# Kernel optimization log

Hardware: AMD Instinct MI355X
Metric: run time of the kernel (lower is better)

Reference implementation:

```python
import jax, jax.numpy as jnp
import numpy as np

N, E = 20000, 320000
H1, C1 = 8, 128   # gat1 heads/out
H2, C2 = 1, 128   # gat2 heads/out
D_IN = 768
NEG_SLOPE = 0.2
BN_EPS = 1e-5


def setup_inputs() -> dict:
    key = jax.random.key(0)
    ks = jax.random.split(key, 16)
    def rn(k, shape, fan):
        return jax.random.normal(k, shape, dtype=jnp.float32) / np.sqrt(fan)
    x = jax.random.normal(ks[0], (N, D_IN), dtype=jnp.float32)
    edge_index = jax.random.randint(ks[1], (2, E), 0, N, dtype=jnp.int64)
    return {
        "x": x,
        "edge_index": edge_index,
        "W1": rn(ks[2], (D_IN, H1 * C1), D_IN),
        "att_src1": rn(ks[3], (H1, C1), C1),
        "att_dst1": rn(ks[4], (H1, C1), C1),
        "b1": jnp.zeros((H1 * C1,), jnp.float32),
        "W2": rn(ks[5], (H1 * C1, H2 * C2), H1 * C1),
        "att_src2": rn(ks[6], (H2, C2), C2),
        "att_dst2": rn(ks[7], (H2, C2), C2),
        "b2": jnp.zeros((C2,), jnp.float32),
        "g1": jnp.ones((H1 * C1,), jnp.float32),
        "be1": jnp.zeros((H1 * C1,), jnp.float32),
        "g2": jnp.ones((C2,), jnp.float32),
        "be2": jnp.zeros((C2,), jnp.float32),
        "Wc1": rn(ks[8], (C2, 64), C2),
        "bc1": jnp.zeros((64,), jnp.float32),
        "Wc2": rn(ks[9], (64, 2), 64),
        "bc2": jnp.zeros((2,), jnp.float32),
    }


def gat_conv(x, src, dst, W, att_src, att_dst, bias, heads, ch, concat):
    n = x.shape[0]
    h = (x @ W).reshape(n, heads, ch)                      # [N,H,C]
    a_s = jnp.sum(h * att_src[None], axis=-1)              # [N,H]
    a_d = jnp.sum(h * att_dst[None], axis=-1)
    e = a_s[src] + a_d[dst]                                # [Et,H]
    e = jax.nn.leaky_relu(e, NEG_SLOPE)
    # segment softmax over incoming edges of each dst node
    m = jax.ops.segment_max(e, dst, num_segments=n)
    ex = jnp.exp(e - m[dst])
    z = jax.ops.segment_sum(ex, dst, num_segments=n)
    alpha = ex / z[dst]                                    # [Et,H]
    msg = alpha[:, :, None] * h[src]                       # [Et,H,C]
    out = jax.ops.segment_sum(msg, dst, num_segments=n)    # [N,H,C]
    if concat:
        out = out.reshape(n, heads * ch)
    else:
        out = out.mean(axis=1)
    return out + bias


def batch_norm(x, gamma, beta):
    mu = x.mean(axis=0)
    var = x.var(axis=0)
    return (x - mu) * jax.lax.rsqrt(var + BN_EPS) * gamma + beta


def reference(x, edge_index, W1, att_src1, att_dst1, b1, W2, att_src2, att_dst2, b2,
              g1, be1, g2, be2, Wc1, bc1, Wc2, bc2):
    n = x.shape[0]
    loop = jnp.arange(n, dtype=edge_index.dtype)
    src = jnp.concatenate([edge_index[0], loop])  # PyG add_self_loops default
    dst = jnp.concatenate([edge_index[1], loop])
    h = gat_conv(x, src, dst, W1, att_src1, att_dst1, b1, H1, C1, True)
    h = jax.nn.elu(batch_norm(h, g1, be1))
    h = gat_conv(h, src, dst, W2, att_src2, att_dst2, b2, H2, C2, False)
    h = jax.nn.elu(batch_norm(h, g2, be2))
    h = jax.nn.relu(h @ Wc1 + bc1)
    return h @ Wc2 + bc2
```

## Files before the change

kernel.cpp:

```cpp
#include <hip/hip_runtime.h>
#include <hip/hip_bf16.h>
#include <math.h>

#define N_NODES 20000
#define N_EDGES 320000
#define DIN 768
#define F1 1024
#define H1 8
#define C1 128
#define F2 128
#define NEG_SLOPE 0.2f
#define BN_EPS 1e-5f
#define RESCALE_THR 8.0f

typedef __attribute__((ext_vector_type(8))) __bf16 bf16x8;
typedef __attribute__((ext_vector_type(4))) float f32x4;

__device__ __forceinline__ float leaky(float x) { return x > 0.f ? x : NEG_SLOPE * x; }

__device__ __forceinline__ unsigned short f2bu(float x) {
  __hip_bfloat16 b = __float2bfloat16(x);
  return *(unsigned short*)&b;
}
__device__ __forceinline__ float b2f(unsigned short u) {
  return __uint_as_float(((unsigned)u) << 16);
}
__device__ __forceinline__ unsigned pack2(float lo, float hi) {
  return (unsigned)f2bu(lo) | ((unsigned)f2bu(hi) << 16);
}

__device__ __forceinline__ void async_copy16(void* lds, const void* g) {
  __builtin_amdgcn_global_load_lds(
      (const __attribute__((address_space(1))) unsigned int*)g,
      (__attribute__((address_space(3))) unsigned int*)lds, 16, 0, 0);
}

__global__ void repack_kernel(const int* raw, int* ei32) {
  int is64 = (raw[1] == 0 && raw[3] == 0 && raw[5] == 0 && raw[7] == 0) ? 1 : 0;
  int e = blockIdx.x * blockDim.x + threadIdx.x;
  if (e < 2 * N_EDGES) {
    ei32[e] = is64 ? raw[2 * e] : raw[e];
  }
}

__global__ void hist_kernel(const int* ei, int* deg) {
  int e = blockIdx.x * blockDim.x + threadIdx.x;
  if (e < N_EDGES) atomicAdd(&deg[ei[N_EDGES + e]], 1);
}

#define NPT 20
__global__ __launch_bounds__(1024) void scan_kernel(const int* __restrict__ deg,
                                                    int* __restrict__ off,
                                                    int* __restrict__ cursor) {
  __shared__ int wsum[16];
  int tid = threadIdx.x;
  int lane = tid & 63, wv = tid >> 6;
  int base = tid * NPT;
  int loc[NPT];
  int run = 0;
#pragma unroll
  for (int k = 0; k < NPT; ++k) {
    int i = base + k;
    int v = (i < N_NODES) ? deg[i] : 0;
    loc[k] = run;
    run += v;
  }
  int incl = run;
  for (int sh = 1; sh < 64; sh <<= 1) {
    int t = __shfl_up(incl, sh, 64);
    if (lane >= sh) incl += t;
  }
  if (lane == 63) wsum[wv] = incl;
  __syncthreads();
  if (wv == 0 && lane < 16) {
    int v = wsum[lane];
    for (int sh = 1; sh < 16; sh <<= 1) {
      int t = __shfl_up(v, sh, 16);
      if (lane >= sh) v += t;
    }
    wsum[lane] = v;
  }
  __syncthreads();
  int wbase = (wv > 0) ? wsum[wv - 1] : 0;
  int tbase = wbase + incl - run;
#pragma unroll
  for (int k = 0; k < NPT; ++k) {
    int i = base + k;
    if (i < N_NODES) {
      int o = tbase + loc[k];
      off[i] = o;
      cursor[i] = o;
    }
  }
  if (tid == 1023) off[N_NODES] = wbase + incl;
}

__global__ void scatter_kernel(const int* ei, int* cursor, int* elist) {
  int e = blockIdx.x * blockDim.x + threadIdx.x;
  if (e < N_EDGES) {
    int dst = ei[N_EDGES + e];
    int p = atomicAdd(&cursor[dst], 1);
    elist[p] = ei[e];
  }
}

__global__ void f2b_kernel(const float* __restrict__ in, unsigned short* __restrict__ out,
                           size_t n4) {
  size_t i = (size_t)blockIdx.x * blockDim.x + threadIdx.x;
  size_t stride = (size_t)gridDim.x * blockDim.x;
  for (; i < n4; i += stride) {
    float4 v = ((const float4*)in)[i];
    ushort4 u;
    u.x = f2bu(v.x); u.y = f2bu(v.y); u.z = f2bu(v.z); u.w = f2bu(v.w);
    ((ushort4*)out)[i] = u;
  }
}

__global__ void transpose_b_kernel(const float* __restrict__ W, unsigned short* __restrict__ WT,
                                   int K, int N) {
  __shared__ float t[32][33];
  int k0 = blockIdx.y * 32, n0 = blockIdx.x * 32;
  int tx = threadIdx.x & 31, ty = threadIdx.x >> 5;
  for (int i = 0; i < 32; i += 8)
    t[ty + i][tx] = W[(size_t)(k0 + ty + i) * N + n0 + tx];
  __syncthreads();
  for (int i = 0; i < 32; i += 8)
    WT[(size_t)(n0 + ty + i) * K + k0 + tx] = f2bu(t[tx][ty + i]);
}

#define GBM 128
#define GBN 128
#define GBK 64
template <int H>
__global__ __launch_bounds__(256) void mfma_gemm_att_kernel(
    const unsigned short* __restrict__ A,
    const unsigned short* __restrict__ BT,
    unsigned short* __restrict__ C,
    const float* __restrict__ att_src,
    const float* __restrict__ att_dst,
    float* __restrict__ as_out,
    float* __restrict__ ad_out,
    int M, int N, int K) {
  __shared__ __hip_bfloat16 As[GBM][GBK];
  __shared__ __hip_bfloat16 Bs[GBN][GBK];
  __shared__ float sred[128][2];
  __shared__ float dred[128][2];
  int tid = threadIdx.x;
  int lane = tid & 63, wid = tid >> 6;
  int wr = wid >> 1, wc = wid & 1;
  int row0 = blockIdx.y * GBM, col0 = blockIdx.x * GBN;
  int head = blockIdx.x;
  int l16 = lane & 15, l4 = lane >> 4;
  f32x4 acc[4][4] = {};
  for (int k0 = 0; k0 < K; k0 += GBK) {
#pragma unroll
    for (int j = 0; j < 4; ++j) {
      int c = j * 256 + tid;
      int r = c >> 3, kk = (c & 7) << 3;
      int ga = row0 + r; if (ga >= M) ga = M - 1;
      async_copy16(&As[r][kk], A + (size_t)ga * K + k0 + kk);
      async_copy16(&Bs[r][kk], BT + (size_t)(col0 + r) * K + k0 + kk);
    }
    __syncthreads();
#pragma unroll
    for (int ks = 0; ks < 2; ++ks) {
      bf16x8 af[4], bfr[4];
#pragma unroll
      for (int i = 0; i < 4; ++i)
        af[i] = *(const bf16x8*)&As[wr * 64 + i * 16 + l16][ks * 32 + l4 * 8];
#pragma unroll
      for (int j = 0; j < 4; ++j)
        bfr[j] = *(const bf16x8*)&Bs[wc * 64 + j * 16 + l16][ks * 32 + l4 * 8];
#pragma unroll
      for (int i = 0; i < 4; ++i)
#pragma unroll
        for (int j = 0; j < 4; ++j)
          acc[i][j] = __builtin_amdgcn_mfma_f32_16x16x32_bf16(af[i], bfr[j], acc[i][j], 0, 0, 0);
    }
    __syncthreads();
  }
#pragma unroll
  for (int i = 0; i < 4; ++i) {
#pragma unroll
    for (int j = 0; j < 4; ++j) {
#pragma unroll
      for (int r = 0; r < 4; ++r) {
        int row = row0 + wr * 64 + i * 16 + l4 * 4 + r;
        int col = col0 + wc * 64 + j * 16 + l16;
        if (row < M) C[(size_t)row * N + col] = f2bu(acc[i][j][r]);
      }
    }
  }
  float avs[4], avd[4];
#pragma unroll
  for (int j = 0; j < 4; ++j) {
    int col = col0 + wc * 64 + j * 16 + l16;
    avs[j] = att_src[col];
    avd[j] = att_dst[col];
  }
#pragma unroll
  for (int i = 0; i < 4; ++i) {
#pragma unroll
    for (int r = 0; r < 4; ++r) {
      float ps = 0.f, pd = 0.f;
#pragma unroll
      for (int j = 0; j < 4; ++j) { ps += acc[i][j][r] * avs[j]; pd += acc[i][j][r] * avd[j]; }
#pragma unroll
      for (int mk = 1; mk < 16; mk <<= 1) {
        ps += __shfl_xor(ps, mk, 64);
        pd += __shfl_xor(pd, mk, 64);
      }
      if (l16 == 0) {
        int lr = wr * 64 + i * 16 + l4 * 4 + r;
        sred[lr][wc] = ps;
        dred[lr][wc] = pd;
      }
    }
  }
  __syncthreads();
  if (tid < 128) {
    int row = row0 + tid;
    if (row < M) {
      as_out[(size_t)row * H + head] = sred[tid][0] + sred[tid][1];
      ad_out[(size_t)row * H + head] = dred[tid][0] + dred[tid][1];
    }
  }
}

__global__ __launch_bounds__(128) void gather1_kernel(const unsigned short* __restrict__ h1,
                                                      const float* __restrict__ as1,
                                                      const float* __restrict__ ad1,
                                                      const int* __restrict__ off,
                                                      const int* __restrict__ elist,
                                                      const float* __restrict__ b1,
                                                      unsigned short* __restrict__ out1) {
  int node = blockIdx.x;
  int tid = threadIdx.x;
  int head = tid >> 4;
  float ad = ad1[node * H1 + head];
  int s = off[node], e = off[node + 1];
  float m = leaky(as1[node * H1 + head] + ad);
  float z = 1.f;
  float acc[8];
  {
    uint4 u = *(const uint4*)(h1 + (size_t)node * F1 + tid * 8);
    acc[0] = __uint_as_float(u.x << 16); acc[1] = __uint_as_float(u.x & 0xffff0000u);
    acc[2] = __uint_as_float(u.y << 16); acc[3] = __uint_as_float(u.y & 0xffff0000u);
    acc[4] = __uint_as_float(u.z << 16); acc[5] = __uint_as_float(u.z & 0xffff0000u);
    acc[6] = __uint_as_float(u.w << 16); acc[7] = __uint_as_float(u.w & 0xffff0000u);
  }
  int src_n = 0; float e_n = 0.f;
  if (s < e) { src_n = elist[s]; e_n = leaky(as1[src_n * H1 + head] + ad); }
  for (int i = s; i < e; ++i) {
    int src = src_n;
    float el = e_n;
    if (i + 1 < e) { src_n = elist[i + 1]; e_n = leaky(as1[src_n * H1 + head] + ad); }
    float w;
    if (el > m + RESCALE_THR) {
      float r = __expf(m - el);
      z *= r;
#pragma unroll
      for (int k = 0; k < 8; ++k) acc[k] *= r;
      m = el;
      w = 1.f;
    } else {
      w = __expf(el - m);
    }
    z += w;
    uint4 u = *(const uint4*)(h1 + (size_t)src * F1 + tid * 8);
    acc[0] += w * __uint_as_float(u.x << 16); acc[1] += w * __uint_as_float(u.x & 0xffff0000u);
    acc[2] += w * __uint_as_float(u.y << 16); acc[3] += w * __uint_as_float(u.y & 0xffff0000u);
    acc[4] += w * __uint_as_float(u.z << 16); acc[5] += w * __uint_as_float(u.z & 0xffff0000u);
    acc[6] += w * __uint_as_float(u.w << 16); acc[7] += w * __uint_as_float(u.w & 0xffff0000u);
  }
  float inv = 1.f / z;
  const float4 bv0 = *(const float4*)(b1 + tid * 8);
  const float4 bv1 = *(const float4*)(b1 + tid * 8 + 4);
  uint4 o;
  o.x = pack2(acc[0] * inv + bv0.x, acc[1] * inv + bv0.y);
  o.y = pack2(acc[2] * inv + bv0.z, acc[3] * inv + bv0.w);
  o.z = pack2(acc[4] * inv + bv1.x, acc[5] * inv + bv1.y);
  o.w = pack2(acc[6] * inv + bv1.z, acc[7] * inv + bv1.w);
  *(uint4*)(out1 + (size_t)node * F1 + tid * 8) = o;
}

__global__ void bnstats_bf16_kernel(const unsigned short* __restrict__ x,
                                    float* __restrict__ sums,
                                    int nrows, int F, int rowsPerBlock) {
  int tid = threadIdx.x;
  int c = tid * 4;
  int r0 = blockIdx.x * rowsPerBlock;
  int rend = min(r0 + rowsPerBlock, nrows);
  float s0 = 0.f, s1 = 0.f, s2 = 0.f, s3 = 0.f;
  float q0 = 0.f, q1 = 0.f, q2 = 0.f, q3 = 0.f;
  for (int r = r0; r < rend; ++r) {
    ushort4 u = *(const ushort4*)(x + (size_t)r * F + c);
    float v0 = b2f(u.x), v1 = b2f(u.y), v2 = b2f(u.z), v3 = b2f(u.w);
    s0 += v0; s1 += v1; s2 += v2; s3 += v3;
    q0 += v0 * v0; q1 += v1 * v1; q2 += v2 * v2; q3 += v3 * v3;
  }
  atomicAdd(&sums[c + 0], s0); atomicAdd(&sums[c + 1], s1);
  atomicAdd(&sums[c + 2], s2); atomicAdd(&sums[c + 3], s3);
  atomicAdd(&sums[F + c + 0], q0); atomicAdd(&sums[F + c + 1], q1);
  atomicAdd(&sums[F + c + 2], q2); atomicAdd(&sums[F + c + 3], q3);
}

template <int CPT>
__global__ void bnstats_kernel(const float* __restrict__ x, float* __restrict__ sums,
                               int nrows, int F, int rowsPerBlock) {
  int tid = threadIdx.x;
  int r0 = blockIdx.x * rowsPerBlock;
  int rend = min(r0 + rowsPerBlock, nrows);
  float s[CPT], q[CPT];
#pragma unroll
  for (int k = 0; k < CPT; ++k) { s[k] = 0.f; q[k] = 0.f; }
  for (int r = r0; r < rend; ++r) {
    const float* row = x + (size_t)r * F;
#pragma unroll
    for (int k = 0; k < CPT; ++k) {
      float v = row[tid + k * blockDim.x];
      s[k] += v; q[k] += v * v;
    }
  }
#pragma unroll
  for (int k = 0; k < CPT; ++k) {
    atomicAdd(&sums[tid + k * blockDim.x], s[k]);
    atomicAdd(&sums[F + tid + k * blockDim.x], q[k]);
  }
}

__global__ void bnfinal_kernel(const float* __restrict__ sums, const float* __restrict__ g,
                               const float* __restrict__ be, float* __restrict__ ss, int F) {
  int c = blockIdx.x * blockDim.x + threadIdx.x;
  if (c < F) {
    float mu = sums[c] * (1.f / N_NODES);
    float var = sums[F + c] * (1.f / N_NODES) - mu * mu;
    float sc = g[c] * rsqrtf(var + BN_EPS);
    ss[c] = sc;
    ss[F + c] = be[c] - mu * sc;
  }
}

__global__ void bnapply_bf16_kernel(unsigned short* __restrict__ x, const float* __restrict__ ss,
                                    int F, size_t total4) {
  size_t i = (size_t)blockIdx.x * blockDim.x + threadIdx.x;
  size_t stride = (size_t)gridDim.x * blockDim.x;
  for (; i < total4; i += stride) {
    int c = (int)((i * 4) & (size_t)(F - 1));
    ushort4 u = ((ushort4*)x)[i];
    float v0 = b2f(u.x) * ss[c + 0] + ss[F + c + 0];
    float v1 = b2f(u.y) * ss[c + 1] + ss[F + c + 1];
    float v2 = b2f(u.z) * ss[c + 2] + ss[F + c + 2];
    float v3 = b2f(u.w) * ss[c + 3] + ss[F + c + 3];
    v0 = v0 > 0.f ? v0 : expm1f(v0);
    v1 = v1 > 0.f ? v1 : expm1f(v1);
    v2 = v2 > 0.f ? v2 : expm1f(v2);
    v3 = v3 > 0.f ? v3 : expm1f(v3);
    u.x = f2bu(v0); u.y = f2bu(v1); u.z = f2bu(v2); u.w = f2bu(v3);
    ((ushort4*)x)[i] = u;
  }
}

__global__ void bnapply_kernel(float* __restrict__ x, const float* __restrict__ ss,
                               int F, size_t total4) {
  size_t i = (size_t)blockIdx.x * blockDim.x + threadIdx.x;
  size_t stride = (size_t)gridDim.x * blockDim.x;
  for (; i < total4; i += stride) {
    int c = (int)((i * 4) & (size_t)(F - 1));
    float4 v = ((float4*)x)[i];
    v.x = v.x * ss[c + 0] + ss[F + c + 0];
    v.y = v.y * ss[c + 1] + ss[F + c + 1];
    v.z = v.z * ss[c + 2] + ss[F + c + 2];
    v.w = v.w * ss[c + 3] + ss[F + c + 3];
    v.x = v.x > 0.f ? v.x : expm1f(v.x);
    v.y = v.y > 0.f ? v.y : expm1f(v.y);
    v.z = v.z > 0.f ? v.z : expm1f(v.z);
    v.w = v.w > 0.f ? v.w : expm1f(v.w);
    ((float4*)x)[i] = v;
  }
}

__global__ __launch_bounds__(64) void gather2_kernel(const unsigned short* __restrict__ h2,
                                                     const float* __restrict__ as2,
                                                     const float* __restrict__ ad2,
                                                     const int* __restrict__ off,
                                                     const int* __restrict__ elist,
                                                     const float* __restrict__ b2,
                                                     float* __restrict__ out2) {
  int node = blockIdx.x;
  int tid = threadIdx.x;
  float ad = ad2[node];
  int s = off[node], e = off[node + 1];
  float m = leaky(as2[node] + ad);
  float z = 1.f;
  float a0, a1;
  {
    unsigned u = *(const unsigned*)(h2 + (size_t)node * F2 + tid * 2);
    a0 = __uint_as_float(u << 16); a1 = __uint_as_float(u & 0xffff0000u);
  }
  int src_n = 0; float e_n = 0.f;
  if (s < e) { src_n = elist[s]; e_n = leaky(as2[src_n] + ad); }
  for (int i = s; i < e; ++i) {
    int src = src_n;
    float el = e_n;
    if (i + 1 < e) { src_n = elist[i + 1]; e_n = leaky(as2[src_n] + ad); }
    float w;
    if (el > m + RESCALE_THR) {
      float r = __expf(m - el);
      z *= r; a0 *= r; a1 *= r;
      m = el; w = 1.f;
    } else {
      w = __expf(el - m);
    }
    z += w;
    unsigned u = *(const unsigned*)(h2 + (size_t)src * F2 + tid * 2);
    a0 += w * __uint_as_float(u << 16);
    a1 += w * __uint_as_float(u & 0xffff0000u);
  }
  float inv = 1.f / z;
  float2 o = make_float2(a0 * inv + b2[tid * 2 + 0], a1 * inv + b2[tid * 2 + 1]);
  *(float2*)(out2 + (size_t)node * F2 + tid * 2) = o;
}

__global__ __launch_bounds__(64) void cls_kernel(const float* __restrict__ h,
                                                 const float* __restrict__ Wc1,
                                                 const float* __restrict__ bc1,
                                                 const float* __restrict__ Wc2,
                                                 const float* __restrict__ bc2,
                                                 float* __restrict__ out) {
  __shared__ float hl[128];
  int node = blockIdx.x;
  int tid = threadIdx.x;
  hl[tid] = h[(size_t)node * F2 + tid];
  hl[tid + 64] = h[(size_t)node * F2 + 64 + tid];
  __syncthreads();
  float acc = bc1[tid];
#pragma unroll
  for (int k = 0; k < 128; ++k) acc += hl[k] * Wc1[k * 64 + tid];
  acc = fmaxf(acc, 0.f);
  float2 w = *(const float2*)(Wc2 + tid * 2);
  float o0 = acc * w.x, o1 = acc * w.y;
  for (int sh = 32; sh >= 1; sh >>= 1) {
    o0 += __shfl_down(o0, sh, 64);
    o1 += __shfl_down(o1, sh, 64);
  }
  if (tid == 0) {
    out[node * 2 + 0] = o0 + bc2[0];
    out[node * 2 + 1] = o1 + bc2[1];
  }
}

extern "C" void kernel_launch(void* const* d_in, const int* in_sizes, int n_in,
                              void* d_out, int out_size, void* d_ws, size_t ws_size,
                              hipStream_t stream) {
  const float* x        = (const float*)d_in[0];
  const int*   ei_raw   = (const int*)d_in[1];
  const float* W1       = (const float*)d_in[2];
  const float* att_src1 = (const float*)d_in[3];
  const float* att_dst1 = (const float*)d_in[4];
  const float* b1       = (const float*)d_in[5];
  const float* W2       = (const float*)d_in[6];
  const float* att_src2 = (const float*)d_in[7];
  const float* att_dst2 = (const float*)d_in[8];
  const float* b2       = (const float*)d_in[9];
  const float* g1       = (const float*)d_in[10];
  const float* be1      = (const float*)d_in[11];
  const float* g2       = (const float*)d_in[12];
  const float* be2      = (const float*)d_in[13];
  const float* Wc1      = (const float*)d_in[14];
  const float* bc1      = (const float*)d_in[15];
  const float* Wc2      = (const float*)d_in[16];
  const float* bc2      = (const float*)d_in[17];
  float* out = (float*)d_out;

  char* ws = (char*)d_ws;
  size_t o = 0;
  unsigned short* h1b   = (unsigned short*)(ws + o); o += (size_t)N_NODES * F1 * 2;
  unsigned short* out1b = (unsigned short*)(ws + o); o += (size_t)N_NODES * F1 * 2;
  unsigned short* xb    = (unsigned short*)(ws + o); o += (size_t)N_NODES * DIN * 2;
  unsigned short* h2b   = (unsigned short*)(ws + o); o += (size_t)N_NODES * F2 * 2;
  float* out2  = (float*)(ws + o); o += (size_t)N_NODES * F2 * 4;
  float* as1   = (float*)(ws + o); o += (size_t)N_NODES * H1 * 4;
  float* ad1   = (float*)(ws + o); o += (size_t)N_NODES * H1 * 4;
  float* as2   = (float*)(ws + o); o += (size_t)N_NODES * 4;
  float* ad2   = (float*)(ws + o); o += (size_t)N_NODES * 4;
  char*  zbase = ws + o;
  float* bnsum1 = (float*)(ws + o); o += F1 * 2 * 4;
  float* bnsum2 = (float*)(ws + o); o += F2 * 2 * 4;
  int*   deg    = (int*)(ws + o); o += (size_t)N_NODES * 4;
  size_t zbytes = (size_t)((ws + o) - zbase);
  int*   offv   = (int*)(ws + o); o += (size_t)(N_NODES + 4) * 4;
  int*   cursor = (int*)(ws + o); o += (size_t)N_NODES * 4;
  int*   elist  = (int*)(ws + o); o += (size_t)N_EDGES * 4;
  float* ss1    = (float*)(ws + o); o += F1 * 2 * 4;
  float* ss2    = (float*)(ws + o); o += F2 * 2 * 4;
  int*   ei32   = (int*)(ws + o); o += (size_t)2 * N_EDGES * 4;
  unsigned short* W1T = (unsigned short*)(ws + o); o += (size_t)F1 * DIN * 2;
  unsigned short* W2T = (unsigned short*)(ws + o); o += (size_t)F2 * F1 * 2;
  (void)ws_size; (void)in_sizes; (void)n_in; (void)out_size;

  hipMemsetAsync((void*)zbase, 0, zbytes, stream);

  f2b_kernel<<<2048, 256, 0, stream>>>(x, xb, (size_t)N_NODES * DIN / 4);
  {
    dim3 g1d(F1 / 32, DIN / 32);
    transpose_b_kernel<<<g1d, 256, 0, stream>>>(W1, W1T, DIN, F1);
    dim3 g2d(F2 / 32, F1 / 32);
    transpose_b_kernel<<<g2d, 256, 0, stream>>>(W2, W2T, F1, F2);
  }

  repack_kernel<<<(2 * N_EDGES + 255) / 256, 256, 0, stream>>>(ei_raw, ei32);
  hist_kernel<<<(N_EDGES + 255) / 256, 256, 0, stream>>>(ei32, deg);
  scan_kernel<<<1, 1024, 0, stream>>>(deg, offv, cursor);
  scatter_kernel<<<(N_EDGES + 255) / 256, 256, 0, stream>>>(ei32, cursor, elist);

  {
    dim3 grid(F1 / GBN, (N_NODES + GBM - 1) / GBM);
    mfma_gemm_att_kernel<H1><<<grid, 256, 0, stream>>>(
        xb, W1T, h1b, att_src1, att_dst1, as1, ad1, N_NODES, F1, DIN);
  }
  gather1_kernel<<<N_NODES, 128, 0, stream>>>(h1b, as1, ad1, offv, elist, b1, out1b);
  {
    int rows = 79;
    int grid = (N_NODES + rows - 1) / rows;
    bnstats_bf16_kernel<<<grid, 256, 0, stream>>>(out1b, bnsum1, N_NODES, F1, rows);
  }
  bnfinal_kernel<<<(F1 + 255) / 256, 256, 0, stream>>>(bnsum1, g1, be1, ss1, F1);
  bnapply_bf16_kernel<<<2048, 256, 0, stream>>>(out1b, ss1, F1, (size_t)N_NODES * F1 / 4);

  {
    dim3 grid(F2 / GBN, (N_NODES + GBM - 1) / GBM);
    mfma_gemm_att_kernel<1><<<grid, 256, 0, stream>>>(
        out1b, W2T, h2b, att_src2, att_dst2, as2, ad2, N_NODES, F2, F1);
  }
  gather2_kernel<<<N_NODES, 64, 0, stream>>>(h2b, as2, ad2, offv, elist, b2, out2);
  {
    int rows = 79;
    int grid = (N_NODES + rows - 1) / rows;
    bnstats_kernel<1><<<grid, 128, 0, stream>>>(out2, bnsum2, N_NODES, F2, rows);
  }
  bnfinal_kernel<<<1, F2, 0, stream>>>(bnsum2, g2, be2, ss2, F2);
  bnapply_kernel<<<1024, 256, 0, stream>>>(out2, ss2, F2, (size_t)N_NODES * F2 / 4);

  cls_kernel<<<N_NODES, 64, 0, stream>>>(out2, Wc1, bc1, Wc2, bc2, out);
}
```

Before: 452.3 us.

## Prefetch gathered rows two edges ahead, fuse histogram and BN2 apply

The gather kernels for both GAT layers now software-pipeline the neighbor loop. The feature row for the edge two steps ahead and the index and attention score for the edge three steps ahead are loaded early, which hides global-memory latency behind the accumulation. The edge repack and degree histogram become one kernel, and the second batch-norm apply plus ELU moves into the classifier kernel, removing two launches and one full pass over the layer-2 output. The cost is more registers in gather1, which may lower occupancy.

New measurement: 429.6 us. 5.0% less time.

```diff
diff --git a/kernel.cpp b/kernel.cpp
--- a/kernel.cpp
+++ b/kernel.cpp
@@ -35,17 +35,14 @@
       (__attribute__((address_space(3))) unsigned int*)lds, 16, 0, 0);
 }
 
-__global__ void repack_kernel(const int* raw, int* ei32) {
+__global__ void repack_hist_kernel(const int* raw, int* ei32, int* deg) {
   int is64 = (raw[1] == 0 && raw[3] == 0 && raw[5] == 0 && raw[7] == 0) ? 1 : 0;
   int e = blockIdx.x * blockDim.x + threadIdx.x;
   if (e < 2 * N_EDGES) {
-    ei32[e] = is64 ? raw[2 * e] : raw[e];
-  }
-}
-
-__global__ void hist_kernel(const int* ei, int* deg) {
-  int e = blockIdx.x * blockDim.x + threadIdx.x;
-  if (e < N_EDGES) atomicAdd(&deg[ei[N_EDGES + e]], 1);
+    int v = is64 ? raw[2 * e] : raw[e];
+    ei32[e] = v;
+    if (e >= N_EDGES) atomicAdd(&deg[v], 1);
+  }
 }
 
 #define NPT 20
@@ -237,7 +234,7 @@
   int node = blockIdx.x;
   int tid = threadIdx.x;
   int head = tid >> 4;
-  float ad = ad1[node * H1 + head];
+  const float ad = ad1[node * H1 + head];
   int s = off[node], e = off[node + 1];
   float m = leaky(as1[node * H1 + head] + ad);
   float z = 1.f;
@@ -249,12 +246,29 @@
     acc[4] = __uint_as_float(u.z << 16); acc[5] = __uint_as_float(u.z & 0xffff0000u);
     acc[6] = __uint_as_float(u.w << 16); acc[7] = __uint_as_float(u.w & 0xffff0000u);
   }
-  int src_n = 0; float e_n = 0.f;
-  if (s < e) { src_n = elist[s]; e_n = leaky(as1[src_n * H1 + head] + ad); }
+  int sB = 0, sC = 0;
+  float eA = 0.f, eB = 0.f, eC = 0.f;
+  uint4 rA = {}, rB = {};
+  if (s < e) {
+    int sA = elist[s];
+    eA = leaky(as1[sA * H1 + head] + ad);
+    rA = *(const uint4*)(h1 + (size_t)sA * F1 + tid * 8);
+  }
+  if (s + 1 < e) {
+    sB = elist[s + 1];
+    eB = leaky(as1[sB * H1 + head] + ad);
+    rB = *(const uint4*)(h1 + (size_t)sB * F1 + tid * 8);
+  }
+  if (s + 2 < e) {
+    sC = elist[s + 2];
+    eC = leaky(as1[sC * H1 + head] + ad);
+  }
   for (int i = s; i < e; ++i) {
-    int src = src_n;
-    float el = e_n;
-    if (i + 1 < e) { src_n = elist[i + 1]; e_n = leaky(as1[src_n * H1 + head] + ad); }
+    uint4 u = rA; float el = eA;
+    rA = rB; eA = eB;
+    sB = sC; eB = eC;
+    if (i + 2 < e) rB = *(const uint4*)(h1 + (size_t)sB * F1 + tid * 8);
+    if (i + 3 < e) { sC = elist[i + 3]; eC = leaky(as1[sC * H1 + head] + ad); }
     float w;
     if (el > m + RESCALE_THR) {
       float r = __expf(m - el);
@@ -267,7 +281,6 @@
       w = __expf(el - m);
     }
     z += w;
-    uint4 u = *(const uint4*)(h1 + (size_t)src * F1 + tid * 8);
     acc[0] += w * __uint_as_float(u.x << 16); acc[1] += w * __uint_as_float(u.x & 0xffff0000u);
     acc[2] += w * __uint_as_float(u.y << 16); acc[3] += w * __uint_as_float(u.y & 0xffff0000u);
     acc[4] += w * __uint_as_float(u.z << 16); acc[5] += w * __uint_as_float(u.z & 0xffff0000u);
@@ -361,25 +374,6 @@
   }
 }
 
-__global__ void bnapply_kernel(float* __restrict__ x, const float* __restrict__ ss,
-                               int F, size_t total4) {
-  size_t i = (size_t)blockIdx.x * blockDim.x + threadIdx.x;
-  size_t stride = (size_t)gridDim.x * blockDim.x;
-  for (; i < total4; i += stride) {
-    int c = (int)((i * 4) & (size_t)(F - 1));
-    float4 v = ((float4*)x)[i];
-    v.x = v.x * ss[c + 0] + ss[F + c + 0];
-    v.y = v.y * ss[c + 1] + ss[F + c + 1];
-    v.z = v.z * ss[c + 2] + ss[F + c + 2];
-    v.w = v.w * ss[c + 3] + ss[F + c + 3];
-    v.x = v.x > 0.f ? v.x : expm1f(v.x);
-    v.y = v.y > 0.f ? v.y : expm1f(v.y);
-    v.z = v.z > 0.f ? v.z : expm1f(v.z);
-    v.w = v.w > 0.f ? v.w : expm1f(v.w);
-    ((float4*)x)[i] = v;
-  }
-}
-
 __global__ __launch_bounds__(64) void gather2_kernel(const unsigned short* __restrict__ h2,
                                                      const float* __restrict__ as2,
                                                      const float* __restrict__ ad2,
@@ -389,7 +383,7 @@
                                                      float* __restrict__ out2) {
   int node = blockIdx.x;
   int tid = threadIdx.x;
-  float ad = ad2[node];
+  const float ad = ad2[node];
   int s = off[node], e = off[node + 1];
   float m = leaky(as2[node] + ad);
   float z = 1.f;
@@ -398,12 +392,29 @@
     unsigned u = *(const unsigned*)(h2 + (size_t)node * F2 + tid * 2);
     a0 = __uint_as_float(u << 16); a1 = __uint_as_float(u & 0xffff0000u);
   }
-  int src_n = 0; float e_n = 0.f;
-  if (s < e) { src_n = elist[s]; e_n = leaky(as2[src_n] + ad); }
+  int sB = 0, sC = 0;
+  float eA = 0.f, eB = 0.f, eC = 0.f;
+  unsigned rA = 0, rB = 0;
+  if (s < e) {
+    int sA = elist[s];
+    eA = leaky(as2[sA] + ad);
+    rA = *(const unsigned*)(h2 + (size_t)sA * F2 + tid * 2);
+  }
+  if (s + 1 < e) {
+    sB = elist[s + 1];
+    eB = leaky(as2[sB] + ad);
+    rB = *(const unsigned*)(h2 + (size_t)sB * F2 + tid * 2);
+  }
+  if (s + 2 < e) {
+    sC = elist[s + 2];
+    eC = leaky(as2[sC] + ad);
+  }
   for (int i = s; i < e; ++i) {
-    int src = src_n;
-    float el = e_n;
-    if (i + 1 < e) { src_n = elist[i + 1]; e_n = leaky(as2[src_n] + ad); }
+    unsigned u = rA; float el = eA;
+    rA = rB; eA = eB;
+    sB = sC; eB = eC;
+    if (i + 2 < e) rB = *(const unsigned*)(h2 + (size_t)sB * F2 + tid * 2);
+    if (i + 3 < e) { sC = elist[i + 3]; eC = leaky(as2[sC] + ad); }
     float w;
     if (el > m + RESCALE_THR) {
       float r = __expf(m - el);
@@ -413,7 +424,6 @@
       w = __expf(el - m);
     }
     z += w;
-    unsigned u = *(const unsigned*)(h2 + (size_t)src * F2 + tid * 2);
     a0 += w * __uint_as_float(u << 16);
     a1 += w * __uint_as_float(u & 0xffff0000u);
   }
@@ -423,6 +433,7 @@
 }
 
 __global__ __launch_bounds__(64) void cls_kernel(const float* __restrict__ h,
+                                                 const float* __restrict__ ss2,
                                                  const float* __restrict__ Wc1,
                                                  const float* __restrict__ bc1,
                                                  const float* __restrict__ Wc2,
@@ -431,8 +442,14 @@
   __shared__ float hl[128];
   int node = blockIdx.x;
   int tid = threadIdx.x;
-  hl[tid] = h[(size_t)node * F2 + tid];
-  hl[tid + 64] = h[(size_t)node * F2 + 64 + tid];
+  {
+    float v = h[(size_t)node * F2 + tid] * ss2[tid] + ss2[F2 + tid];
+    v = v > 0.f ? v : expm1f(v);
+    hl[tid] = v;
+    float v2 = h[(size_t)node * F2 + 64 + tid] * ss2[64 + tid] + ss2[F2 + 64 + tid];
+    v2 = v2 > 0.f ? v2 : expm1f(v2);
+    hl[tid + 64] = v2;
+  }
   __syncthreads();
   float acc = bc1[tid];
 #pragma unroll
@@ -509,8 +526,7 @@
     transpose_b_kernel<<<g2d, 256, 0, stream>>>(W2, W2T, F1, F2);
   }
 
-  repack_kernel<<<(2 * N_EDGES + 255) / 256, 256, 0, stream>>>(ei_raw, ei32);
-  hist_kernel<<<(N_EDGES + 255) / 256, 256, 0, stream>>>(ei32, deg);
+  repack_hist_kernel<<<(2 * N_EDGES + 255) / 256, 256, 0, stream>>>(ei_raw, ei32, deg);
   scan_kernel<<<1, 1024, 0, stream>>>(deg, offv, cursor);
   scatter_kernel<<<(N_EDGES + 255) / 256, 256, 0, stream>>>(ei32, cursor, elist);
 
@@ -540,7 +556,6 @@
     bnstats_kernel<1><<<grid, 128, 0, stream>>>(out2, bnsum2, N_NODES, F2, rows);
   }
   bnfinal_kernel<<<1, F2, 0, stream>>>(bnsum2, g2, be2, ss2, F2);
-  bnapply_kernel<<<1024, 256, 0, stream>>>(out2, ss2, F2, (size_t)N_NODES * F2 / 4);
-
-  cls_kernel<<<N_NODES, 64, 0, stream>>>(out2, Wc1, bc1, Wc2, bc2, out);
-}
+
+  cls_kernel<<<N_NODES, 64, 0, stream>>>(out2, ss2, Wc1, bc1, Wc2, bc2, out);
+}
```
